# Performance work log

Hardware: AMD Instinct MI355X
Metric: run time of the kernel (lower is better)

Reference implementation:

```python
import jax, jax.numpy as jnp
import numpy as np

N, E, H = 50000, 800000, 128
HQ = H // 4  # 32


def _mlp(x, w1, b1, w2, b2):
    return jax.nn.relu(x @ w1 + b1) @ w2 + b2


def setup_inputs() -> dict:
    key = jax.random.key(0)
    ks = jax.random.split(key, 16)

    def lin(k, fan_in, fan_out):
        lim = 1.0 / np.sqrt(fan_in)
        kw, kb = jax.random.split(k)
        w = jax.random.uniform(kw, (fan_in, fan_out), jnp.float32, -lim, lim)
        b = jax.random.uniform(kb, (fan_out,), jnp.float32, -lim, lim)
        return w, b

    x = jax.random.normal(ks[0], (N, H), jnp.float32)
    pos = jax.random.normal(ks[1], (N, 3), jnp.float32)
    edge_index = jax.random.randint(ks[2], (2, E), 0, N, jnp.int64)

    pw1, pb1 = lin(ks[3], 3, HQ)
    pw2, pb2 = lin(ks[4], HQ, HQ)
    mw1, mb1 = lin(ks[5], 2 * H + HQ, H)
    mw2, mb2 = lin(ks[6], H, H)
    uw1, ub1 = lin(ks[7], 2 * H, H)
    uw2, ub2 = lin(ks[8], H, H)

    return dict(x=x, pos=pos, edge_index=edge_index,
                pw1=pw1, pb1=pb1, pw2=pw2, pb2=pb2,
                mw1=mw1, mb1=mb1, mw2=mw2, mb2=mb2,
                uw1=uw1, ub1=ub1, uw2=uw2, ub2=ub2)


def reference(x, pos, edge_index,
              pw1, pb1, pw2, pb2,
              mw1, mb1, mw2, mb2,
              uw1, ub1, uw2, ub2):
    row, col = edge_index[0], edge_index[1]
    # position features from relative positions [E, 3] -> [E, H//4]
    pos_feat = _mlp(pos[row] - pos[col], pw1, pb1, pw2, pb2)
    # per-edge messages [E, 2H + H//4] -> [E, H]
    msg_in = jnp.concatenate([x[row], x[col], pos_feat], axis=-1)
    messages = _mlp(msg_in, mw1, mb1, mw2, mb2)
    # scatter-add messages into destination nodes (index_add on col)
    agg = jax.ops.segment_sum(messages, col, num_segments=x.shape[0])
    # node update [N, 2H] -> [N, H]
    return _mlp(jnp.concatenate([x, agg], axis=-1), uw1, ub1, uw2, ub2)
```

## Files before the change

kernel.cpp:

```cpp
#include <hip/hip_runtime.h>
#include <hip/hip_bf16.h>

#define NN 50000
#define NE 800000
#define HD 128
#define SCAN_CHUNK 1024
#define SCAN_BLOCKS ((NN + SCAN_CHUNK - 1) / SCAN_CHUNK)

typedef __attribute__((ext_vector_type(8))) short s16x8;
typedef __attribute__((ext_vector_type(4))) float f32x4;

static __device__ __forceinline__ unsigned short f2bf(float f) {
    unsigned int u = __float_as_uint(f);
    u = (u + 0x7FFFu + ((u >> 16) & 1u)) >> 16;
    return (unsigned short)u;
}
static __device__ __forceinline__ float bf2f(unsigned short h) {
    return __uint_as_float(((unsigned int)h) << 16);
}
static __device__ __forceinline__ unsigned int f2bf2(float lo, float hi) {
    __hip_bfloat162 h = __float22bfloat162_rn(make_float2(lo, hi));
    return *reinterpret_cast<unsigned int*>(&h);
}

#define WFENCE() do { asm volatile("s_waitcnt lgkmcnt(0)" ::: "memory"); \
                      __builtin_amdgcn_sched_barrier(0); } while (0)

__global__ void prep_kernel(const float* __restrict__ pw2, const float* __restrict__ pb2,
                            const float* __restrict__ mw1, const float* __restrict__ mb1,
                            float* __restrict__ Wpc, float* __restrict__ bc)
{
    int tid = threadIdx.x;
    for (int idx = tid; idx < 32 * 128; idx += 256) {
        int j = idx >> 7, k = idx & 127;
        float s = 0.f;
        #pragma unroll 8
        for (int i = 0; i < 32; ++i) s += pw2[j * 32 + i] * mw1[(256 + i) * 128 + k];
        Wpc[idx] = s;
    }
    if (tid < 128) {
        float s = mb1[tid];
        #pragma unroll 8
        for (int i = 0; i < 32; ++i) s += pb2[i] * mw1[(256 + i) * 128 + tid];
        bc[tid] = s;
    }
}

__global__ void hist_kernel(const int* __restrict__ ei, int* __restrict__ cnt)
{
    __shared__ int sIdx64;
    if (threadIdx.x == 0) {
        int z = 1;
        for (int k = 0; k < 16; ++k) if (ei[2 * k + 1] != 0) z = 0;
        sIdx64 = z;
    }
    __syncthreads();
    int g = blockIdx.x * 256 + threadIdx.x;
    if (g >= NE / 2) return;
    int e0 = g * 2;
    int c0, c1;
    if (sIdx64) { int4 q = *(const int4*)&ei[2 * NE + 2 * e0]; c0 = q.x; c1 = q.z; }
    else        { int2 q = *(const int2*)&ei[NE + e0];         c0 = q.x; c1 = q.y; }
    atomicAdd(&cnt[c0], 1);
    atomicAdd(&cnt[c1], 1);
}

__global__ void scan1_kernel(const int* __restrict__ cnt, int* __restrict__ cursor,
                             int* __restrict__ bsum)
{
    __shared__ int tot[256];
    int b = blockIdx.x, t = threadIdx.x;
    int i0 = b * SCAN_CHUNK + t * 4;
    int v[4];
    #pragma unroll
    for (int k = 0; k < 4; ++k) v[k] = (i0 + k < NN) ? cnt[i0 + k] : 0;
    tot[t] = v[0] + v[1] + v[2] + v[3];
    __syncthreads();
    if (t == 0) {
        int run = 0;
        for (int i = 0; i < 256; ++i) { int x = tot[i]; tot[i] = run; run += x; }
        bsum[b] = run;
    }
    __syncthreads();
    int p = tot[t];
    #pragma unroll
    for (int k = 0; k < 4; ++k) {
        if (i0 + k < NN) cursor[i0 + k] = p;
        p += v[k];
    }
}

__global__ void scan2_kernel(int* __restrict__ bsum)
{
    if (threadIdx.x == 0) {
        int run = 0;
        for (int i = 0; i < SCAN_BLOCKS; ++i) { int x = bsum[i]; bsum[i] = run; run += x; }
    }
}

__global__ void scan3_kernel(int* __restrict__ cursor, const int* __restrict__ bsum)
{
    int b = blockIdx.x, t = threadIdx.x;
    int carry = bsum[b];
    int i0 = b * SCAN_CHUNK + t * 4;
    #pragma unroll
    for (int k = 0; k < 4; ++k)
        if (i0 + k < NN) cursor[i0 + k] += carry;
}

__global__ void scatter_kernel(const int* __restrict__ ei,
                               int* __restrict__ cursor, int2* __restrict__ sRC)
{
    __shared__ int sIdx64;
    if (threadIdx.x == 0) {
        int z = 1;
        for (int k = 0; k < 16; ++k) if (ei[2 * k + 1] != 0) z = 0;
        sIdx64 = z;
    }
    __syncthreads();
    int g = blockIdx.x * 256 + threadIdx.x;
    if (g >= NE / 2) return;
    int e0 = g * 2;
    int r0, r1, c0, c1;
    if (sIdx64) {
        int4 qr = *(const int4*)&ei[2 * e0];           r0 = qr.x; r1 = qr.z;
        int4 qc = *(const int4*)&ei[2 * NE + 2 * e0];  c0 = qc.x; c1 = qc.z;
    } else {
        int2 qr = *(const int2*)&ei[e0];       r0 = qr.x; r1 = qr.y;
        int2 qc = *(const int2*)&ei[NE + e0];  c0 = qc.x; c1 = qc.y;
    }
    int p0 = atomicAdd(&cursor[c0], 1);
    sRC[p0] = make_int2(r0, c0);
    int p1 = atomicAdd(&cursor[c1], 1);
    sRC[p1] = make_int2(r1, c1);
}

__global__ __launch_bounds__(256, 2) void node_pre_kernel(
    const float* __restrict__ x, const float* __restrict__ mw1,
    const float* __restrict__ bcv,
    unsigned short* __restrict__ xa, unsigned short* __restrict__ xb)
{
    __shared__ __align__(16) unsigned short sB[256 * 136];
    __shared__ __align__(16) unsigned short sSt[4][16 * 64];

    int tid = threadIdx.x;
    for (int idx = tid; idx < 256 * 128; idx += 256) {
        int c = idx & 255, k = idx >> 8;
        float v = (c < 128) ? mw1[k * 128 + c] : mw1[(128 + k) * 128 + (c - 128)];
        sB[c * 136 + k] = f2bf(v);
    }
    __syncthreads();

    int lane = tid & 63, wv = tid >> 6;
    int r16 = lane & 15, g4 = lane >> 4;
    unsigned short* st = sSt[wv];
    float bcx[8];
    #pragma unroll
    for (int i = 0; i < 8; ++i) bcx[i] = bcv[i * 16 + r16];
    const int NT = NN / 16;

    for (int t = blockIdx.x * 4 + wv; t < NT; t += gridDim.x * 4) {
        int r0 = t * 16;
        int row = r0 + r16;
        s16x8 a[4];
        #pragma unroll
        for (int ks = 0; ks < 4; ++ks) {
            const float* p = &x[(size_t)row * HD + ks * 32 + g4 * 8];
            float4 v0 = *(const float4*)p;
            float4 v1 = *(const float4*)(p + 4);
            union { s16x8 v; unsigned int u[4]; } av;
            av.u[0] = f2bf2(v0.x, v0.y); av.u[1] = f2bf2(v0.z, v0.w);
            av.u[2] = f2bf2(v1.x, v1.y); av.u[3] = f2bf2(v1.z, v1.w);
            a[ks] = av.v;
        }
        #pragma unroll
        for (int grp = 0; grp < 4; ++grp) {
            #pragma unroll
            for (int tc2 = 0; tc2 < 4; ++tc2) {
                int tc = grp * 4 + tc2;
                int col = tc * 16 + r16;
                f32x4 acc = {0.f, 0.f, 0.f, 0.f};
                #pragma unroll
                for (int ks = 0; ks < 4; ++ks) {
                    s16x8 b = *(const s16x8*)&sB[col * 136 + ks * 32 + g4 * 8];
                    acc = __builtin_amdgcn_mfma_f32_16x16x32_bf16(a[ks], b, acc, 0, 0, 0);
                }
                float badd = (grp >= 2) ? bcx[(grp - 2) * 4 + tc2] : 0.f;
                #pragma unroll
                for (int j = 0; j < 4; ++j)
                    st[(g4 * 4 + j) * 64 + tc2 * 16 + r16] = f2bf(acc[j] + badd);
            }
            WFENCE();
            unsigned short* dst = (grp < 2) ? xa : xb;
            int ch = (grp & 1) * 64;
            #pragma unroll
            for (int i = 0; i < 2; ++i) {
                int idx = i * 512 + lane * 8;
                int rr = idx >> 6, cc = idx & 63;
                *(s16x8*)&dst[(size_t)(r0 + rr) * HD + ch + cc] = *(const s16x8*)&st[idx];
            }
            WFENCE();
        }
    }
}

__global__ __launch_bounds__(256, 3) void edge_kernel(
    const float* __restrict__ pos, const int2* __restrict__ sRC,
    const float* __restrict__ pw1, const float* __restrict__ pb1,
    const unsigned short* __restrict__ xa, const unsigned short* __restrict__ xb,
    const float* __restrict__ Wpc,
    float* __restrict__ aggH)
{
    __shared__ __align__(16) unsigned short sT[4][16 * 136];
    __shared__ int sECs[4][16];

    int tid = threadIdx.x;
    int lane = tid & 63, wv = tid >> 6;
    int r16 = lane & 15, g4 = lane >> 4;
    unsigned short* stg = sT[wv];
    int* secw = sECs[wv];

    s16x8 wr[8];
    #pragma unroll
    for (int tc = 0; tc < 8; ++tc) {
        s16x8 w;
        #pragma unroll
        for (int i = 0; i < 8; ++i)
            w[i] = (short)f2bf(Wpc[(g4 * 8 + i) * 128 + tc * 16 + r16]);
        wr[tc] = w;
    }
    float pw10[8], pw11[8], pw12[8], pb1r[8];
    #pragma unroll
    for (int i = 0; i < 8; ++i) {
        int k = g4 * 8 + i;
        pw10[i] = pw1[k]; pw11[i] = pw1[32 + k]; pw12[i] = pw1[64 + k];
        pb1r[i] = pb1[k];
    }

    const int NW = gridDim.x * 4;
    const int NT = NE / 16;
    int gw = blockIdx.x * 4 + wv;
    if (gw >= NT) return;

    int2 rc = sRC[gw * 16 + r16];
    int2 rcN = rc;
    if (gw + NW < NT) rcN = sRC[(gw + NW) * 16 + r16];
    float dp0 = pos[rc.x * 3 + 0] - pos[rc.y * 3 + 0];
    float dp1 = pos[rc.x * 3 + 1] - pos[rc.y * 3 + 1];
    float dp2 = pos[rc.x * 3 + 2] - pos[rc.y * 3 + 2];
    s16x8 ga[4], gb[4];
    #pragma unroll
    for (int s = 0; s < 4; ++s) {
        int gx = __shfl(rc.x, s * 4 + g4, 64);
        int gy = __shfl(rc.y, s * 4 + g4, 64);
        ga[s] = *(const s16x8*)&xa[(size_t)gx * HD + r16 * 8];
        gb[s] = *(const s16x8*)&xb[(size_t)gy * HD + r16 * 8];
    }

    for (int t = gw; t < NT; t += NW) {
        bool hn  = (t + NW) < NT;
        bool hn2 = (t + 2 * NW) < NT;

        #pragma unroll
        for (int s = 0; s < 4; ++s) {
            union { s16x8 v; unsigned int u[4]; } o;
            #pragma unroll
            for (int i2 = 0; i2 < 4; ++i2) {
                float v0 = bf2f((unsigned short)ga[s][2 * i2]) +
                           bf2f((unsigned short)gb[s][2 * i2]);
                float v1 = bf2f((unsigned short)ga[s][2 * i2 + 1]) +
                           bf2f((unsigned short)gb[s][2 * i2 + 1]);
                o.u[i2] = f2bf2(v0, v1);
            }
            *(s16x8*)&stg[(s * 4 + g4) * 136 + r16 * 8] = o.v;
        }
        if (lane < 16) secw[lane] = rc.y;
        WFENCE();

        if (hn) {
            #pragma unroll
            for (int s = 0; s < 4; ++s) {
                int gx = __shfl(rcN.x, s * 4 + g4, 64);
                int gy = __shfl(rcN.y, s * 4 + g4, 64);
                ga[s] = *(const s16x8*)&xa[(size_t)gx * HD + r16 * 8];
                gb[s] = *(const s16x8*)&xb[(size_t)gy * HD + r16 * 8];
            }
        }

        int2 rcN2 = rcN;
        if (hn2) rcN2 = sRC[(t + 2 * NW) * 16 + r16];

        float dp0N = 0.f, dp1N = 0.f, dp2N = 0.f;
        if (hn) {
            dp0N = pos[rcN.x * 3 + 0] - pos[rcN.y * 3 + 0];
            dp1N = pos[rcN.x * 3 + 1] - pos[rcN.y * 3 + 1];
            dp2N = pos[rcN.x * 3 + 2] - pos[rcN.y * 3 + 2];
        }

        union { s16x8 v; unsigned int u[4]; } apf;
        #pragma unroll
        for (int i2 = 0; i2 < 4; ++i2) {
            int i = 2 * i2;
            float v0 = fmaf(dp0, pw10[i], fmaf(dp1, pw11[i], fmaf(dp2, pw12[i], pb1r[i])));
            float v1 = fmaf(dp0, pw10[i+1], fmaf(dp1, pw11[i+1], fmaf(dp2, pw12[i+1], pb1r[i+1])));
            apf.u[i2] = f2bf2(fmaxf(v0, 0.f), fmaxf(v1, 0.f));
        }

        #pragma unroll
        for (int tc = 0; tc < 8; ++tc) {
            f32x4 z = {0.f, 0.f, 0.f, 0.f};
            f32x4 a1 = __builtin_amdgcn_mfma_f32_16x16x32_bf16(apf.v, wr[tc], z, 0, 0, 0);
            #pragma unroll
            for (int j = 0; j < 4; ++j) {
                int e = g4 * 4 + j, col = tc * 16 + r16;
                float v = a1[j] + bf2f(stg[e * 136 + col]);
                stg[e * 136 + col] = f2bf(fmaxf(v, 0.f));
            }
        }
        WFENCE();

        {
            int f0 = lane, f1 = lane + 64;
            int cur = secw[0];
            float run0 = bf2f(stg[f0]);
            float run1 = bf2f(stg[f1]);
            #pragma unroll
            for (int e = 1; e < 16; ++e) {
                int c = secw[e];
                float v0 = bf2f(stg[e * 136 + f0]);
                float v1 = bf2f(stg[e * 136 + f1]);
                if (c != cur) {
                    unsafeAtomicAdd(&aggH[(size_t)cur * HD + f0], run0);
                    unsafeAtomicAdd(&aggH[(size_t)cur * HD + f1], run1);
                    cur = c; run0 = v0; run1 = v1;
                } else { run0 += v0; run1 += v1; }
            }
            unsafeAtomicAdd(&aggH[(size_t)cur * HD + f0], run0);
            unsafeAtomicAdd(&aggH[(size_t)cur * HD + f1], run1);
        }
        WFENCE();

        rc = rcN; rcN = rcN2; dp0 = dp0N; dp1 = dp1N; dp2 = dp2N;
    }
}

__global__ __launch_bounds__(256, 2) void aggmm_kernel(
    const float* __restrict__ aggH, const int* __restrict__ cnt,
    const float* __restrict__ mw2, const float* __restrict__ mb2,
    unsigned short* __restrict__ agg2)
{
    __shared__ __align__(16) unsigned short sB[128 * 136];
    __shared__ __align__(16) unsigned short sSt[4][16 * 64];

    int tid = threadIdx.x;
    for (int idx = tid; idx < 128 * 128; idx += 256) {
        int c = idx & 127, k = idx >> 7;
        sB[c * 136 + k] = f2bf(mw2[k * 128 + c]);
    }
    __syncthreads();

    int lane = tid & 63, wv = tid >> 6;
    int r16 = lane & 15, g4 = lane >> 4;
    unsigned short* st = sSt[wv];
    float mb2r[8];
    #pragma unroll
    for (int tc = 0; tc < 8; ++tc) mb2r[tc] = mb2[tc * 16 + r16];

    const int NT = NN / 16;
    for (int t = blockIdx.x * 4 + wv; t < NT; t += gridDim.x * 4) {
        int r0 = t * 16;
        int row = r0 + r16;
        s16x8 a[4];
        #pragma unroll
        for (int ks = 0; ks < 4; ++ks) {
            const float* p = &aggH[(size_t)row * HD + ks * 32 + g4 * 8];
            float4 v0 = *(const float4*)p;
            float4 v1 = *(const float4*)(p + 4);
            union { s16x8 v; unsigned int u[4]; } av;
            av.u[0] = f2bf2(v0.x, v0.y); av.u[1] = f2bf2(v0.z, v0.w);
            av.u[2] = f2bf2(v1.x, v1.y); av.u[3] = f2bf2(v1.z, v1.w);
            a[ks] = av.v;
        }
        float cn[4];
        #pragma unroll
        for (int j = 0; j < 4; ++j) cn[j] = (float)cnt[r0 + g4 * 4 + j];
        #pragma unroll
        for (int half = 0; half < 2; ++half) {
            #pragma unroll
            for (int tc2 = 0; tc2 < 4; ++tc2) {
                int tc = half * 4 + tc2;
                int col = tc * 16 + r16;
                f32x4 acc;
                #pragma unroll
                for (int j = 0; j < 4; ++j) acc[j] = cn[j] * mb2r[tc];
                #pragma unroll
                for (int ks = 0; ks < 4; ++ks) {
                    s16x8 b = *(const s16x8*)&sB[col * 136 + ks * 32 + g4 * 8];
                    acc = __builtin_amdgcn_mfma_f32_16x16x32_bf16(a[ks], b, acc, 0, 0, 0);
                }
                #pragma unroll
                for (int j = 0; j < 4; ++j)
                    st[(g4 * 4 + j) * 64 + tc2 * 16 + r16] = f2bf(acc[j]);
            }
            WFENCE();
            #pragma unroll
            for (int i = 0; i < 2; ++i) {
                int idx = i * 512 + lane * 8;
                int rr = idx >> 6, cc = idx & 63;
                *(s16x8*)&agg2[(size_t)(r0 + rr) * HD + half * 64 + cc] = *(const s16x8*)&st[idx];
            }
            WFENCE();
        }
    }
}

__global__ __launch_bounds__(512, 2) void upd_kernel(
    const float* __restrict__ x, const unsigned short* __restrict__ agg2,
    const float* __restrict__ uw1, const float* __restrict__ ub1,
    const float* __restrict__ uw2, const float* __restrict__ ub2,
    float* __restrict__ out)
{
    __shared__ __align__(16) unsigned short sB1[128 * 264];
    __shared__ __align__(16) unsigned short sB2[128 * 136];
    __shared__ __align__(16) unsigned short sSt[8][16 * 136];

    int tid = threadIdx.x;
    for (int idx = tid; idx < 256 * 128; idx += 512) {
        int c = idx & 127, k = idx >> 7;
        sB1[c * 264 + k] = f2bf(uw1[k * 128 + c]);
    }
    for (int idx = tid; idx < 128 * 128; idx += 512) {
        int c = idx & 127, k = idx >> 7;
        sB2[c * 136 + k] = f2bf(uw2[k * 128 + c]);
    }
    __syncthreads();

    int lane = tid & 63, wv = tid >> 6;
    int r16 = lane & 15, g4 = lane >> 4;
    unsigned short* st = sSt[wv];
    float ub1r[8], ub2r[8];
    #pragma unroll
    for (int tc = 0; tc < 8; ++tc) {
        ub1r[tc] = ub1[tc * 16 + r16];
        ub2r[tc] = ub2[tc * 16 + r16];
    }

    const int NT = NN / 16;
    for (int t = blockIdx.x * 8 + wv; t < NT; t += gridDim.x * 8) {
        int r0 = t * 16;
        int row = r0 + r16;
        s16x8 a[8];
        #pragma unroll
        for (int ks = 0; ks < 4; ++ks) {
            const float* p = &x[(size_t)row * HD + ks * 32 + g4 * 8];
            float4 v0 = *(const float4*)p;
            float4 v1 = *(const float4*)(p + 4);
            union { s16x8 v; unsigned int u[4]; } av;
            av.u[0] = f2bf2(v0.x, v0.y); av.u[1] = f2bf2(v0.z, v0.w);
            av.u[2] = f2bf2(v1.x, v1.y); av.u[3] = f2bf2(v1.z, v1.w);
            a[ks] = av.v;
        }
        #pragma unroll
        for (int ks = 4; ks < 8; ++ks)
            a[ks] = *(const s16x8*)&agg2[(size_t)row * HD + (ks - 4) * 32 + g4 * 8];

        #pragma unroll
        for (int tc = 0; tc < 8; ++tc) {
            int col = tc * 16 + r16;
            float bv = ub1r[tc];
            f32x4 acc = {bv, bv, bv, bv};
            #pragma unroll
            for (int ks = 0; ks < 8; ++ks) {
                s16x8 b = *(const s16x8*)&sB1[col * 264 + ks * 32 + g4 * 8];
                acc = __builtin_amdgcn_mfma_f32_16x16x32_bf16(a[ks], b, acc, 0, 0, 0);
            }
            #pragma unroll
            for (int j = 0; j < 4; ++j)
                st[(g4 * 4 + j) * 136 + col] = f2bf(fmaxf(acc[j], 0.f));
        }
        WFENCE();
        s16x8 a2[4];
        #pragma unroll
        for (int ks = 0; ks < 4; ++ks)
            a2[ks] = *(const s16x8*)&st[r16 * 136 + ks * 32 + g4 * 8];
        WFENCE();
        #pragma unroll
        for (int tc = 0; tc < 8; ++tc) {
            int col = tc * 16 + r16;
            float bv = ub2r[tc];
            f32x4 acc = {bv, bv, bv, bv};
            #pragma unroll
            for (int ks = 0; ks < 4; ++ks) {
                s16x8 b = *(const s16x8*)&sB2[col * 136 + ks * 32 + g4 * 8];
                acc = __builtin_amdgcn_mfma_f32_16x16x32_bf16(a2[ks], b, acc, 0, 0, 0);
            }
            #pragma unroll
            for (int j = 0; j < 4; ++j)
                out[(size_t)(r0 + g4 * 4 + j) * HD + col] = acc[j];
        }
    }
}

extern "C" void kernel_launch(void* const* d_in, const int* in_sizes, int n_in,
                              void* d_out, int out_size, void* d_ws, size_t ws_size,
                              hipStream_t stream)
{
    const float* x   = (const float*)d_in[0];
    const float* pos = (const float*)d_in[1];
    const int*   ei  = (const int*)d_in[2];
    const float* pw1 = (const float*)d_in[3];
    const float* pb1 = (const float*)d_in[4];
    const float* pw2 = (const float*)d_in[5];
    const float* pb2 = (const float*)d_in[6];
    const float* mw1 = (const float*)d_in[7];
    const float* mb1 = (const float*)d_in[8];
    const float* mw2 = (const float*)d_in[9];
    const float* mb2 = (const float*)d_in[10];
    const float* uw1 = (const float*)d_in[11];
    const float* ub1 = (const float*)d_in[12];
    const float* uw2 = (const float*)d_in[13];
    const float* ub2 = (const float*)d_in[14];
    float* out = (float*)d_out;

    char* ws = (char*)d_ws;
    float*          aggH   = (float*)(ws);
    unsigned short* xa     = (unsigned short*)(ws + 25600000);
    unsigned short* xb     = (unsigned short*)(ws + 38400000);
    float*          Wpc    = (float*)(ws + 51200000);
    float*          bcv    = (float*)(ws + 51216384);
    int*            cnt    = (int*)(ws + 51216896);
    int*            cursor = (int*)(ws + 51417600);
    int*            bsum   = (int*)(ws + 51618304);
    int2*           sRC    = (int2*)(ws + 51618560);

    unsigned short* agg2 = xa;

    hipMemsetAsync(aggH, 0, (size_t)NN * HD * sizeof(float), stream);
    hipMemsetAsync(cnt, 0, NN * sizeof(int), stream);
    prep_kernel<<<1, 256, 0, stream>>>(pw2, pb2, mw1, mb1, Wpc, bcv);
    hist_kernel<<<(NE / 2 + 255) / 256, 256, 0, stream>>>(ei, cnt);
    scan1_kernel<<<SCAN_BLOCKS, 256, 0, stream>>>(cnt, cursor, bsum);
    scan2_kernel<<<1, 64, 0, stream>>>(bsum);
    scan3_kernel<<<SCAN_BLOCKS, 256, 0, stream>>>(cursor, bsum);
    scatter_kernel<<<(NE / 2 + 255) / 256, 256, 0, stream>>>(ei, cursor, sRC);
    node_pre_kernel<<<512, 256, 0, stream>>>(x, mw1, bcv, xa, xb);
    edge_kernel<<<768, 256, 0, stream>>>(pos, sRC, pw1, pb1, xa, xb, Wpc, aggH);
    aggmm_kernel<<<512, 256, 0, stream>>>(aggH, cnt, mw2, mb2, agg2);
    upd_kernel<<<256, 512, 0, stream>>>(x, agg2, uw1, ub1, uw2, ub2, out);
}
```

Before: 248.6 us.

## Fold message second layer into update weights and drop aggmm kernel

Precomputes W3 = mw2 · uw1[128:] and b3 = mb2 · uw1[128:] so the update MLP consumes the raw fp32 aggregate directly. The separate aggmm pass, along with its bf16 intermediate round-trip through global memory, is removed. The edge kernel now seeds the MFMA accumulator with the staged pre-activation instead of adding it afterwards, and its occupancy hint and grid size are raised. This changes bf16 rounding points, and the cursor workspace region is reused for W3/b3.

```diff
diff --git a/kernel.cpp b/kernel.cpp
--- a/kernel.cpp
+++ b/kernel.cpp
@@ -43,6 +43,29 @@
         #pragma unroll 8
         for (int i = 0; i < 32; ++i) s += pb2[i] * mw1[(256 + i) * 128 + tid];
         bc[tid] = s;
+    }
+}
+
+__global__ void prep2_kernel(const float* __restrict__ mw2, const float* __restrict__ mb2,
+                             const float* __restrict__ uw1,
+                             float* __restrict__ W3, float* __restrict__ b3)
+{
+    int idx = blockIdx.x * 256 + threadIdx.x;
+    if (idx < 128 * 128) {
+        int k = idx >> 7, j = idx & 127;
+        float s = 0.f;
+        #pragma unroll 4
+        for (int c = 0; c < 128; ++c)
+            s += mw2[k * 128 + c] * uw1[(128 + c) * 128 + j];
+        W3[idx] = s;
+    }
+    if (blockIdx.x == 0 && threadIdx.x < 128) {
+        int j = threadIdx.x;
+        float s = 0.f;
+        #pragma unroll 4
+        for (int c = 0; c < 128; ++c)
+            s += mb2[c] * uw1[(128 + c) * 128 + j];
+        b3[j] = s;
     }
 }
 
@@ -204,7 +227,7 @@
     }
 }
 
-__global__ __launch_bounds__(256, 3) void edge_kernel(
+__global__ __launch_bounds__(256, 5) void edge_kernel(
     const float* __restrict__ pos, const int2* __restrict__ sRC,
     const float* __restrict__ pw1, const float* __restrict__ pb1,
     const unsigned short* __restrict__ xa, const unsigned short* __restrict__ xb,
@@ -308,14 +331,14 @@
 
         #pragma unroll
         for (int tc = 0; tc < 8; ++tc) {
-            f32x4 z = {0.f, 0.f, 0.f, 0.f};
-            f32x4 a1 = __builtin_amdgcn_mfma_f32_16x16x32_bf16(apf.v, wr[tc], z, 0, 0, 0);
-            #pragma unroll
-            for (int j = 0; j < 4; ++j) {
-                int e = g4 * 4 + j, col = tc * 16 + r16;
-                float v = a1[j] + bf2f(stg[e * 136 + col]);
-                stg[e * 136 + col] = f2bf(fmaxf(v, 0.f));
-            }
+            f32x4 acc;
+            #pragma unroll
+            for (int j = 0; j < 4; ++j)
+                acc[j] = bf2f(stg[(g4 * 4 + j) * 136 + tc * 16 + r16]);
+            acc = __builtin_amdgcn_mfma_f32_16x16x32_bf16(apf.v, wr[tc], acc, 0, 0, 0);
+            #pragma unroll
+            for (int j = 0; j < 4; ++j)
+                stg[(g4 * 4 + j) * 136 + tc * 16 + r16] = f2bf(fmaxf(acc[j], 0.f));
         }
         WFENCE();
 
@@ -344,36 +367,48 @@
     }
 }
 
-__global__ __launch_bounds__(256, 2) void aggmm_kernel(
-    const float* __restrict__ aggH, const int* __restrict__ cnt,
-    const float* __restrict__ mw2, const float* __restrict__ mb2,
-    unsigned short* __restrict__ agg2)
-{
-    __shared__ __align__(16) unsigned short sB[128 * 136];
-    __shared__ __align__(16) unsigned short sSt[4][16 * 64];
+__global__ __launch_bounds__(512, 2) void upd_kernel(
+    const float* __restrict__ x, const float* __restrict__ aggH,
+    const int* __restrict__ cnt,
+    const float* __restrict__ uw1, const float* __restrict__ ub1,
+    const float* __restrict__ W3, const float* __restrict__ b3,
+    const float* __restrict__ uw2, const float* __restrict__ ub2,
+    float* __restrict__ out)
+{
+    __shared__ __align__(16) unsigned short sB1a[128 * 136];
+    __shared__ __align__(16) unsigned short sW3l[128 * 136];
+    __shared__ __align__(16) unsigned short sB2[128 * 136];
+    __shared__ __align__(16) unsigned short sSt[8][16 * 136];
 
     int tid = threadIdx.x;
-    for (int idx = tid; idx < 128 * 128; idx += 256) {
+    for (int idx = tid; idx < 128 * 128; idx += 512) {
         int c = idx & 127, k = idx >> 7;
-        sB[c * 136 + k] = f2bf(mw2[k * 128 + c]);
+        sB1a[c * 136 + k] = f2bf(uw1[k * 128 + c]);
+        sW3l[c * 136 + k] = f2bf(W3[k * 128 + c]);
+        sB2[c * 136 + k]  = f2bf(uw2[k * 128 + c]);
     }
     __syncthreads();
 
     int lane = tid & 63, wv = tid >> 6;
     int r16 = lane & 15, g4 = lane >> 4;
     unsigned short* st = sSt[wv];
-    float mb2r[8];
-    #pragma unroll
-    for (int tc = 0; tc < 8; ++tc) mb2r[tc] = mb2[tc * 16 + r16];
+    float ub1r[8], ub2r[8], b3r[8];
+    #pragma unroll
+    for (int tc = 0; tc < 8; ++tc) {
+        ub1r[tc] = ub1[tc * 16 + r16];
+        ub2r[tc] = ub2[tc * 16 + r16];
+        b3r[tc]  = b3[tc * 16 + r16];
+    }
 
     const int NT = NN / 16;
-    for (int t = blockIdx.x * 4 + wv; t < NT; t += gridDim.x * 4) {
+    for (int t = blockIdx.x * 8 + wv; t < NT; t += gridDim.x * 8) {
         int r0 = t * 16;
         int row = r0 + r16;
-        s16x8 a[4];
-        #pragma unroll
-        for (int ks = 0; ks < 4; ++ks) {
-            const float* p = &aggH[(size_t)row * HD + ks * 32 + g4 * 8];
+        s16x8 a[8];
+        #pragma unroll
+        for (int ks = 0; ks < 8; ++ks) {
+            const float* p = (ks < 4) ? &x[(size_t)row * HD + ks * 32 + g4 * 8]
+                                      : &aggH[(size_t)row * HD + (ks - 4) * 32 + g4 * 8];
             float4 v0 = *(const float4*)p;
             float4 v1 = *(const float4*)(p + 4);
             union { s16x8 v; unsigned int u[4]; } av;
@@ -384,94 +419,21 @@
         float cn[4];
         #pragma unroll
         for (int j = 0; j < 4; ++j) cn[j] = (float)cnt[r0 + g4 * 4 + j];
-        #pragma unroll
-        for (int half = 0; half < 2; ++half) {
-            #pragma unroll
-            for (int tc2 = 0; tc2 < 4; ++tc2) {
-                int tc = half * 4 + tc2;
-                int col = tc * 16 + r16;
-                f32x4 acc;
-                #pragma unroll
-                for (int j = 0; j < 4; ++j) acc[j] = cn[j] * mb2r[tc];
-                #pragma unroll
-                for (int ks = 0; ks < 4; ++ks) {
-                    s16x8 b = *(const s16x8*)&sB[col * 136 + ks * 32 + g4 * 8];
-                    acc = __builtin_amdgcn_mfma_f32_16x16x32_bf16(a[ks], b, acc, 0, 0, 0);
-                }
-                #pragma unroll
-                for (int j = 0; j < 4; ++j)
-                    st[(g4 * 4 + j) * 64 + tc2 * 16 + r16] = f2bf(acc[j]);
-            }
-            WFENCE();
-            #pragma unroll
-            for (int i = 0; i < 2; ++i) {
-                int idx = i * 512 + lane * 8;
-                int rr = idx >> 6, cc = idx & 63;
-                *(s16x8*)&agg2[(size_t)(r0 + rr) * HD + half * 64 + cc] = *(const s16x8*)&st[idx];
-            }
-            WFENCE();
-        }
-    }
-}
-
-__global__ __launch_bounds__(512, 2) void upd_kernel(
-    const float* __restrict__ x, const unsigned short* __restrict__ agg2,
-    const float* __restrict__ uw1, const float* __restrict__ ub1,
-    const float* __restrict__ uw2, const float* __restrict__ ub2,
-    float* __restrict__ out)
-{
-    __shared__ __align__(16) unsigned short sB1[128 * 264];
-    __shared__ __align__(16) unsigned short sB2[128 * 136];
-    __shared__ __align__(16) unsigned short sSt[8][16 * 136];
-
-    int tid = threadIdx.x;
-    for (int idx = tid; idx < 256 * 128; idx += 512) {
-        int c = idx & 127, k = idx >> 7;
-        sB1[c * 264 + k] = f2bf(uw1[k * 128 + c]);
-    }
-    for (int idx = tid; idx < 128 * 128; idx += 512) {
-        int c = idx & 127, k = idx >> 7;
-        sB2[c * 136 + k] = f2bf(uw2[k * 128 + c]);
-    }
-    __syncthreads();
-
-    int lane = tid & 63, wv = tid >> 6;
-    int r16 = lane & 15, g4 = lane >> 4;
-    unsigned short* st = sSt[wv];
-    float ub1r[8], ub2r[8];
-    #pragma unroll
-    for (int tc = 0; tc < 8; ++tc) {
-        ub1r[tc] = ub1[tc * 16 + r16];
-        ub2r[tc] = ub2[tc * 16 + r16];
-    }
-
-    const int NT = NN / 16;
-    for (int t = blockIdx.x * 8 + wv; t < NT; t += gridDim.x * 8) {
-        int r0 = t * 16;
-        int row = r0 + r16;
-        s16x8 a[8];
-        #pragma unroll
-        for (int ks = 0; ks < 4; ++ks) {
-            const float* p = &x[(size_t)row * HD + ks * 32 + g4 * 8];
-            float4 v0 = *(const float4*)p;
-            float4 v1 = *(const float4*)(p + 4);
-            union { s16x8 v; unsigned int u[4]; } av;
-            av.u[0] = f2bf2(v0.x, v0.y); av.u[1] = f2bf2(v0.z, v0.w);
-            av.u[2] = f2bf2(v1.x, v1.y); av.u[3] = f2bf2(v1.z, v1.w);
-            a[ks] = av.v;
-        }
-        #pragma unroll
-        for (int ks = 4; ks < 8; ++ks)
-            a[ks] = *(const s16x8*)&agg2[(size_t)row * HD + (ks - 4) * 32 + g4 * 8];
 
         #pragma unroll
         for (int tc = 0; tc < 8; ++tc) {
             int col = tc * 16 + r16;
-            float bv = ub1r[tc];
-            f32x4 acc = {bv, bv, bv, bv};
-            #pragma unroll
-            for (int ks = 0; ks < 8; ++ks) {
-                s16x8 b = *(const s16x8*)&sB1[col * 264 + ks * 32 + g4 * 8];
+            f32x4 acc;
+            #pragma unroll
+            for (int j = 0; j < 4; ++j) acc[j] = ub1r[tc] + cn[j] * b3r[tc];
+            #pragma unroll
+            for (int ks = 0; ks < 4; ++ks) {
+                s16x8 b = *(const s16x8*)&sB1a[col * 136 + ks * 32 + g4 * 8];
+                acc = __builtin_amdgcn_mfma_f32_16x16x32_bf16(a[ks], b, acc, 0, 0, 0);
+            }
+            #pragma unroll
+            for (int ks = 4; ks < 8; ++ks) {
+                s16x8 b = *(const s16x8*)&sW3l[col * 136 + (ks - 4) * 32 + g4 * 8];
                 acc = __builtin_amdgcn_mfma_f32_16x16x32_bf16(a[ks], b, acc, 0, 0, 0);
             }
             #pragma unroll
@@ -533,7 +495,8 @@
     int*            bsum   = (int*)(ws + 51618304);
     int2*           sRC    = (int2*)(ws + 51618560);
 
-    unsigned short* agg2 = xa;
+    float* W3 = (float*)(ws + 51417600);
+    float* b3 = (float*)(ws + 51417600 + 65536);
 
     hipMemsetAsync(aggH, 0, (size_t)NN * HD * sizeof(float), stream);
     hipMemsetAsync(cnt, 0, NN * sizeof(int), stream);
@@ -543,8 +506,8 @@
     scan2_kernel<<<1, 64, 0, stream>>>(bsum);
     scan3_kernel<<<SCAN_BLOCKS, 256, 0, stream>>>(cursor, bsum);
     scatter_kernel<<<(NE / 2 + 255) / 256, 256, 0, stream>>>(ei, cursor, sRC);
+    prep2_kernel<<<64, 256, 0, stream>>>(mw2, mb2, uw1, W3, b3);
     node_pre_kernel<<<512, 256, 0, stream>>>(x, mw1, bcv, xa, xb);
-    edge_kernel<<<768, 256, 0, stream>>>(pos, sRC, pw1, pb1, xa, xb, Wpc, aggH);
-    aggmm_kernel<<<512, 256, 0, stream>>>(aggH, cnt, mw2, mb2, agg2);
-    upd_kernel<<<256, 512, 0, stream>>>(x, agg2, uw1, ub1, uw2, ub2, out);
-}
+    edge_kernel<<<1280, 256, 0, stream>>>(pos, sRC, pw1, pb1, xa, xb, Wpc, aggH);
+    upd_kernel<<<256, 512, 0, stream>>>(x, aggH, cnt, uw1, ub1, W3, b3, uw2, ub2, out);
+}
```

Result: slower. 312.6 us (+25.8%).
